# Kernel optimization log

Hardware: AMD Instinct MI355X
Metric: run time of the kernel (lower is better)

The kernel has to match this reference:

```python
import jax, jax.numpy as jnp
import numpy as np
from jax import lax

GAMMA = 0.001  # init kwarg gamma
DN = ('NCHW', 'OIHW', 'NCHW')


def _maxpool2(x):
    # 2x2 max pool, stride 2, NCHW
    return lax.reduce_window(x, -jnp.inf, lax.max, (1, 1, 2, 2), (1, 1, 2, 2), 'VALID')


def _features(x, w1, b1, w2, b2):
    h = lax.conv_general_dilated(x, w1, (1, 1), 'SAME', dimension_numbers=DN)
    h = _maxpool2(jax.nn.relu(h + b1[None, :, None, None]))
    h = lax.conv_general_dilated(h, w2, (1, 1), 'SAME', dimension_numbers=DN)
    h = _maxpool2(jax.nn.relu(h + b2[None, :, None, None]))
    return h.reshape(h.shape[0], -1)  # [N, 16*7*7=784]


def setup_inputs() -> dict:
    key = jax.random.key(0)
    ks = jax.random.split(key, 7)
    x = jax.random.normal(ks[0], (4096, 1, 28, 28), dtype=jnp.float32)
    w1 = jax.random.normal(ks[1], (8, 1, 3, 3), dtype=jnp.float32) * 0.1
    b1 = jax.random.normal(ks[2], (8,), dtype=jnp.float32) * 0.1
    w2 = jax.random.normal(ks[3], (16, 8, 3, 3), dtype=jnp.float32) * 0.1
    b2 = jax.random.normal(ks[4], (16,), dtype=jnp.float32) * 0.1
    support = jax.random.uniform(ks[5], (8192, 784), dtype=jnp.float32)
    alpha = jax.random.normal(ks[6], (8192, 4), dtype=jnp.float32)
    return {'x': x, 'w1': w1, 'b1': b1, 'w2': w2, 'b2': b2,
            'support': support, 'alpha': alpha}


def reference(x, w1, b1, w2, b2, support, alpha):
    feats = _features(x, w1, b1, w2, b2)                      # [N, 784]
    # Pairwise squared distances via expansion (replaces the N*M python loop)
    f2 = jnp.sum(feats * feats, axis=1, keepdims=True)        # [N, 1]
    s2 = jnp.sum(support * support, axis=1)[None, :]          # [1, M]
    d2 = f2 + s2 - 2.0 * (feats @ support.T)                  # [N, M]
    K = jnp.exp(-GAMMA * d2)                                  # RBF kernel matrix
    return K @ alpha                                          # [N, n_classes]
```

## Files before the change

### kernel.cpp

```cpp
#include <hip/hip_runtime.h>
#include <hip/hip_bf16.h>
#include <cstdint>

#define GAMMA 0.001f
#define TILE_BYTES 114688

typedef __attribute__((ext_vector_type(4))) float f32x4;
typedef __attribute__((ext_vector_type(8))) int v8i;
typedef __attribute__((ext_vector_type(8))) short bh8;
typedef unsigned char u8;

__device__ inline unsigned pack4_fp8(float4 f) {
  unsigned p = __builtin_amdgcn_cvt_pk_fp8_f32(f.x, f.y, 0, false);
  p = __builtin_amdgcn_cvt_pk_fp8_f32(f.z, f.w, p, true);
  return p;
}

__device__ inline ushort bf16u(float v) {
  __hip_bfloat16 h = __float2bfloat16(v);
  return *(ushort*)&h;
}

__global__ __launch_bounds__(256, 4) void conv_prep_kernel(
    const float* __restrict__ x, const float* __restrict__ w1,
    const float* __restrict__ b1, const float* __restrict__ w2,
    const float* __restrict__ b2, const float* __restrict__ support,
    const float* __restrict__ alpha, u8* __restrict__ feats_t,
    u8* __restrict__ sup_t, float* __restrict__ beta,
    float* __restrict__ ef) {
  int tid = threadIdx.x;
  int bx = blockIdx.x;

  if (bx >= 2048) {
    int lane = tid & 63, wave = tid >> 6;
    int m = (bx - 2048) * 4 + wave;
    const float* row = support + (size_t)m * 784;
    int mt = m >> 7, mr = m & 127;
    u8* tb = sup_t + (size_t)mt * TILE_BYTES;
    float ss = 0.f;
    if (lane < 56) {
      uint4 w;
      if (lane < 49) {
        float4 f0 = ((const float4*)row)[lane * 4 + 0];
        float4 f1 = ((const float4*)row)[lane * 4 + 1];
        float4 f2 = ((const float4*)row)[lane * 4 + 2];
        float4 f3 = ((const float4*)row)[lane * 4 + 3];
        ss = f0.x * f0.x + f0.y * f0.y + f0.z * f0.z + f0.w * f0.w +
             f1.x * f1.x + f1.y * f1.y + f1.z * f1.z + f1.w * f1.w +
             f2.x * f2.x + f2.y * f2.y + f2.z * f2.z + f2.w * f2.w +
             f3.x * f3.x + f3.y * f3.y + f3.z * f3.z + f3.w * f3.w;
        w.x = pack4_fp8(f0); w.y = pack4_fp8(f1);
        w.z = pack4_fp8(f2); w.w = pack4_fp8(f3);
      } else {
        w.x = 0; w.y = 0; w.z = 0; w.w = 0;
      }
      int kk = lane >> 3, u = lane & 7, q = u >> 1, h = u & 1;
      int qs = q ^ ((mr >> 1) & 3);
      *(uint4*)(tb + kk * 16384 + h * 8192 + mr * 64 + qs * 16) = w;
    }
#pragma unroll
    for (int s = 1; s < 64; s <<= 1) ss += __shfl_xor(ss, s, 64);
    if (lane == 0) {
      float es = __expf(-GAMMA * ss);
      float4 a = ((const float4*)alpha)[m];
      float4 b;
      b.x = es * a.x; b.y = es * a.y; b.z = es * a.z; b.w = es * a.w;
      ((float4*)beta)[m] = b;
    }
    return;
  }

  __shared__ float xp[2][900];
  __shared__ alignas(16) ushort a1h[2][2048];
  __shared__ float w1s[72], b1s[8], b2s[16];
  __shared__ float w2s[1152];
  __shared__ alignas(8) ushort sc[2][16][212];
  __shared__ alignas(16) u8 fb[2][784];
  __shared__ float red[256];

  int lane = tid & 63, wave = tid >> 6;

  for (int t = tid; t < 1800; t += 256) ((float*)xp)[t] = 0.f;
  for (int t = tid; t < 1024; t += 256) ((uint4*)a1h)[t] = (uint4){0, 0, 0, 0};
  if (tid < 72) w1s[tid] = w1[tid];
  if (tid < 8) b1s[tid] = b1[tid];
  if (tid < 16) b2s[tid] = b2[tid];
  for (int t = tid; t < 1152; t += 256) w2s[t] = w2[t];
  __syncthreads();

  int oc = lane & 15, quad = lane >> 4;
  bh8 wf[3];
#pragma unroll
  for (int g = 0; g < 3; g++) {
    int tap = g * 4 + quad;
#pragma unroll
    for (int j = 0; j < 8; j++) {
      float v = (tap < 9) ? w2s[oc * 72 + j * 9 + tap] : 0.f;
      wf[g][j] = (short)bf16u(v);
    }
  }

  for (int t = tid; t < 392; t += 256) {
    int img = t >= 196, j = t - img * 196;
    float4 v = ((const float4*)(x + (size_t)(bx * 2 + img) * 784))[j];
    int r = j / 7, c = (j % 7) * 4;
    float* p = &xp[img][(r + 1) * 30 + (c + 1)];
    p[0] = v.x; p[1] = v.y; p[2] = v.z; p[3] = v.w;
  }
  __syncthreads();

  for (int idx = tid; idx < 3136; idx += 256) {
    int img = idx >= 1568;
    int rem = idx - img * 1568;
    int c = rem / 196, r2 = rem % 196;
    int ph = r2 / 14, pw = r2 % 14;
    const float* w = &w1s[c * 9];
    const float* xb = &xp[img][(2 * ph) * 30 + (2 * pw)];
    float t[4][4];
#pragma unroll
    for (int a = 0; a < 4; a++) {
      float2 u0 = *(const float2*)(xb + a * 30);
      float2 u1 = *(const float2*)(xb + a * 30 + 2);
      t[a][0] = u0.x; t[a][1] = u0.y; t[a][2] = u1.x; t[a][3] = u1.y;
    }
    float s00 = 0, s01 = 0, s10 = 0, s11 = 0;
#pragma unroll
    for (int dy = 0; dy < 3; dy++)
#pragma unroll
      for (int dx = 0; dx < 3; dx++) {
        float wv = w[dy * 3 + dx];
        s00 += t[dy][dx] * wv;     s01 += t[dy][dx + 1] * wv;
        s10 += t[dy + 1][dx] * wv; s11 += t[dy + 1][dx + 1] * wv;
      }
    float mx = fmaxf(fmaxf(s00, s01), fmaxf(s10, s11));
    float val = fmaxf(mx + b1s[c], 0.f);
    a1h[img][((ph + 1) * 16 + (pw + 1)) * 8 + c] = bf16u(val);
  }
  __syncthreads();

  {
    int img2 = wave >> 1, half = wave & 1;
    int Tstart = half * 7, Tcnt = half ? 6 : 7;
    const ushort* abase = a1h[img2];
    int mrow = lane & 15;
    for (int t = 0; t < Tcnt; ++t) {
      int T = Tstart + t;
      int p = T * 16 + mrow;
      int pc = p > 195 ? 195 : p;
      int y = pc / 14, xq = pc - y * 14;
      int cell = y * 16 + xq;
      f32x4 acc = (f32x4){0, 0, 0, 0};
#pragma unroll
      for (int g = 0; g < 3; g++) {
        int tap = g * 4 + quad;
        const ushort* ap;
        if (g == 2 && quad > 0) {
          ap = abase;
        } else {
          int dy = tap / 3, dx = tap - dy * 3;
          ap = abase + (cell + dy * 16 + dx) * 8;
        }
        bh8 af = *(const bh8*)ap;
        acc = __builtin_amdgcn_mfma_f32_16x16x32_bf16(af, wf[g], acc, 0, 0, 0);
      }
      int pos0 = T * 16 + quad * 4;
      ushort4 s4;
      s4.x = bf16u(acc.x); s4.y = bf16u(acc.y);
      s4.z = bf16u(acc.z); s4.w = bf16u(acc.w);
      *(ushort4*)(&sc[img2][oc][pos0]) = s4;
    }
  }
  __syncthreads();

  int img = tid >> 7, r = tid & 127;
  float fsq = 0.f;
  if (r < 112) {
    int o = r & 15, y7 = r >> 4;
    const ushort* srow = sc[img][o];
    float bo = b2s[o];
#pragma unroll
    for (int x7 = 0; x7 < 7; x7++) {
      int p = 28 * y7 + 2 * x7;
      unsigned u0 = *(const unsigned*)(&srow[p]);
      unsigned u1 = *(const unsigned*)(&srow[p + 14]);
      float a = __uint_as_float(u0 << 16);
      float b = __uint_as_float(u0 & 0xffff0000u);
      float c = __uint_as_float(u1 << 16);
      float d = __uint_as_float(u1 & 0xffff0000u);
      float mx = fmaxf(fmaxf(a, b), fmaxf(c, d));
      float val = fmaxf(mx + bo, 0.f);
      fb[img][o * 49 + y7 * 7 + x7] =
          (u8)(__builtin_amdgcn_cvt_pk_fp8_f32(val, 0.f, 0, false) & 0xff);
      fsq += val * val;
    }
  }
  red[tid] = fsq;
  __syncthreads();
  for (int s = 64; s > 0; s >>= 1) {
    if ((tid & 127) < s) red[tid] += red[tid + s];
    __syncthreads();
  }
  if ((tid & 127) == 0) ef[bx * 2 + img] = __expf(-GAMMA * red[tid]);

  if (tid < 112) {
    int im = tid >= 56, j = tid - im * 56;
    uint4 v;
    if (j < 49) v = ((const uint4*)fb[im])[j];
    else { v.x = 0; v.y = 0; v.z = 0; v.w = 0; }
    int n = bx * 2 + im;
    int nt = n >> 7, nr = n & 127;
    int kk = j >> 3, u = j & 7, q = u >> 1, h = u & 1;
    int qs = q ^ ((nr >> 1) & 3);
    *(uint4*)(feats_t + (size_t)nt * TILE_BYTES + kk * 16384 + h * 8192 +
              nr * 64 + qs * 16) = v;
  }
}

__global__ __launch_bounds__(256, 2) void rbf_gemm_kernel(
    const u8* __restrict__ feats_t, const u8* __restrict__ sup_t,
    const float* __restrict__ beta, float* __restrict__ partial) {
  int tid = threadIdx.x;
  int wave = tid >> 6, lane = tid & 63;
  int bx = blockIdx.x;
  int chunk = bx & 63, nb = bx >> 6;
  int wn = wave >> 1, wm = wave & 1;
  int col = lane & 15, quad = lane >> 4;
  int slot = quad ^ ((col >> 1) & 3);

  const u8* abase = feats_t + (size_t)nb * TILE_BYTES +
                    (wn * 64 + col) * 64 + slot * 16;
  const u8* bbase = sup_t + (size_t)chunk * TILE_BYTES +
                    (wm * 64 + col) * 64 + slot * 16;

  f32x4 acc[4][4];
#pragma unroll
  for (int i = 0; i < 4; i++)
#pragma unroll
    for (int j = 0; j < 4; j++) acc[i][j] = (f32x4){0, 0, 0, 0};

#pragma unroll 2
  for (int kk = 0; kk < 7; ++kk) {
    const u8* ak = abase + kk * 16384;
    const u8* bk = bbase + kk * 16384;
    v8i av[4], bv[4];
#pragma unroll
    for (int i = 0; i < 4; i++) {
      const u8* p = ak + i * 1024;
      int4 lo = *(const int4*)p;
      int4 hi = *(const int4*)(p + 8192);
      av[i] = (v8i){lo.x, lo.y, lo.z, lo.w, hi.x, hi.y, hi.z, hi.w};
    }
#pragma unroll
    for (int j = 0; j < 4; j++) {
      const u8* p = bk + j * 1024;
      int4 lo = *(const int4*)p;
      int4 hi = *(const int4*)(p + 8192);
      bv[j] = (v8i){lo.x, lo.y, lo.z, lo.w, hi.x, hi.y, hi.z, hi.w};
    }
#pragma unroll
    for (int i = 0; i < 4; i++)
#pragma unroll
      for (int j = 0; j < 4; j++)
        acc[i][j] = __builtin_amdgcn_mfma_scale_f32_16x16x128_f8f6f4(
            av[i], bv[j], acc[i][j], 0, 0, 0, 0x7f7f7f7f, 0, 0x7f7f7f7f);
  }

#pragma unroll
  for (int i = 0; i < 4; i++)
#pragma unroll
    for (int j = 0; j < 4; j++) {
      acc[i][j].x = __expf(2.f * GAMMA * acc[i][j].x);
      acc[i][j].y = __expf(2.f * GAMMA * acc[i][j].y);
      acc[i][j].z = __expf(2.f * GAMMA * acc[i][j].z);
      acc[i][j].w = __expf(2.f * GAMMA * acc[i][j].w);
    }
  int n0 = nb * 128, m0 = chunk * 128;
#pragma unroll
  for (int c = 0; c < 4; ++c) {
    float bl[4];
#pragma unroll
    for (int j = 0; j < 4; j++)
      bl[j] = beta[(m0 + wm * 64 + j * 16 + col) * 4 + c];
#pragma unroll
    for (int i = 0; i < 4; i++) {
      f32x4 s = acc[i][0] * bl[0] + acc[i][1] * bl[1] + acc[i][2] * bl[2] +
                acc[i][3] * bl[3];
#pragma unroll
      for (int st = 1; st < 16; st <<= 1) {
        s.x += __shfl_xor(s.x, st, 16);
        s.y += __shfl_xor(s.y, st, 16);
        s.z += __shfl_xor(s.z, st, 16);
        s.w += __shfl_xor(s.w, st, 16);
      }
      if (col == c) {
        int n = n0 + wn * 64 + i * 16 + quad * 4;
        float* pp = partial + (((size_t)chunk * 2 + wm) * 4096 + n) * 4 + c;
        pp[0] = s.x; pp[4] = s.y; pp[8] = s.z; pp[12] = s.w;
      }
    }
  }
}

__global__ __launch_bounds__(256) void reduce_kernel(
    const float* __restrict__ partial, const float* __restrict__ ef,
    float* __restrict__ out) {
  __shared__ float4 sred[4][64];
  int nl = threadIdx.x & 63, chq = threadIdx.x >> 6;
  int n = blockIdx.x * 64 + nl;
  const float4* p = (const float4*)partial;
  float sx = 0, sy = 0, sz = 0, sw = 0;
  for (int ch = chq * 32; ch < chq * 32 + 32; ch++) {
    float4 v = p[(size_t)ch * 4096 + n];
    sx += v.x; sy += v.y; sz += v.z; sw += v.w;
  }
  sred[chq][nl] = (float4){sx, sy, sz, sw};
  __syncthreads();
  if (chq == 0) {
    float4 a = sred[0][nl], b = sred[1][nl], c = sred[2][nl], d = sred[3][nl];
    float e = ef[n];
    float4 o;
    o.x = e * (a.x + b.x + c.x + d.x);
    o.y = e * (a.y + b.y + c.y + d.y);
    o.z = e * (a.z + b.z + c.z + d.z);
    o.w = e * (a.w + b.w + c.w + d.w);
    ((float4*)out)[n] = o;
  }
}

extern "C" void kernel_launch(void* const* d_in, const int* in_sizes, int n_in,
                              void* d_out, int out_size, void* d_ws,
                              size_t ws_size, hipStream_t stream) {
  const float* x = (const float*)d_in[0];
  const float* w1 = (const float*)d_in[1];
  const float* b1 = (const float*)d_in[2];
  const float* w2 = (const float*)d_in[3];
  const float* b2 = (const float*)d_in[4];
  const float* support = (const float*)d_in[5];
  const float* alpha = (const float*)d_in[6];
  float* out = (float*)d_out;

  u8* ws = (u8*)d_ws;
  u8* sup_t = ws;
  u8* feats_t = ws + 7340032;
  float* beta = (float*)(ws + 11010048);
  float* ef = (float*)(ws + 11141120);
  float* partial = (float*)(ws + 11157504);

  conv_prep_kernel<<<4096, 256, 0, stream>>>(x, w1, b1, w2, b2, support, alpha,
                                             feats_t, sup_t, beta, ef);
  rbf_gemm_kernel<<<2048, 256, 0, stream>>>(feats_t, sup_t, beta, partial);
  reduce_kernel<<<64, 256, 0, stream>>>(partial, ef, out);
}
```

Measured before the change: 172.0 us.

## Raise GEMM occupancy with staggered fragment loads and widen final reduction

The RBF GEMM kernel's launch bound goes from 2 to 4 blocks per CU and the k-loop is no longer unrolled. A-fragments are now loaded two at a time, interleaved with the MFMAs, which lowers register pressure and lets more waves hide global-load latency. The reduce kernel now uses 256 blocks of 16 rows, each summing 8 chunks per thread group followed by a shared-memory tree reduction, giving more parallelism for the small final pass. The risk is that forcing 4 blocks per CU could cause spills, and dropping the unroll reduces load/compute overlap within a wave.

```diff
diff --git a/kernel.cpp b/kernel.cpp
--- a/kernel.cpp
+++ b/kernel.cpp
@@ -216,7 +216,7 @@
   }
 }
 
-__global__ __launch_bounds__(256, 2) void rbf_gemm_kernel(
+__global__ __launch_bounds__(256, 4) void rbf_gemm_kernel(
     const u8* __restrict__ feats_t, const u8* __restrict__ sup_t,
     const float* __restrict__ beta, float* __restrict__ partial) {
   int tid = threadIdx.x;
@@ -238,32 +238,47 @@
 #pragma unroll
     for (int j = 0; j < 4; j++) acc[i][j] = (f32x4){0, 0, 0, 0};
 
-#pragma unroll 2
+#define LDFRAG(p)                                                      \
+  ({                                                                   \
+    int4 lo_ = *(const int4*)(p);                                      \
+    int4 hi_ = *(const int4*)((p) + 8192);                             \
+    (v8i){lo_.x, lo_.y, lo_.z, lo_.w, hi_.x, hi_.y, hi_.z, hi_.w};     \
+  })
+#define MFMA(a, b, c)                                                  \
+  __builtin_amdgcn_mfma_scale_f32_16x16x128_f8f6f4(                    \
+      (a), (b), (c), 0, 0, 0, 0x7f7f7f7f, 0, 0x7f7f7f7f)
+
+#pragma unroll 1
   for (int kk = 0; kk < 7; ++kk) {
     const u8* ak = abase + kk * 16384;
     const u8* bk = bbase + kk * 16384;
-    v8i av[4], bv[4];
-#pragma unroll
-    for (int i = 0; i < 4; i++) {
-      const u8* p = ak + i * 1024;
-      int4 lo = *(const int4*)p;
-      int4 hi = *(const int4*)(p + 8192);
-      av[i] = (v8i){lo.x, lo.y, lo.z, lo.w, hi.x, hi.y, hi.z, hi.w};
-    }
-#pragma unroll
-    for (int j = 0; j < 4; j++) {
-      const u8* p = bk + j * 1024;
-      int4 lo = *(const int4*)p;
-      int4 hi = *(const int4*)(p + 8192);
-      bv[j] = (v8i){lo.x, lo.y, lo.z, lo.w, hi.x, hi.y, hi.z, hi.w};
-    }
-#pragma unroll
-    for (int i = 0; i < 4; i++)
-#pragma unroll
-      for (int j = 0; j < 4; j++)
-        acc[i][j] = __builtin_amdgcn_mfma_scale_f32_16x16x128_f8f6f4(
-            av[i], bv[j], acc[i][j], 0, 0, 0, 0x7f7f7f7f, 0, 0x7f7f7f7f);
-  }
+    v8i bv0 = LDFRAG(bk);
+    v8i bv1 = LDFRAG(bk + 1024);
+    v8i bv2 = LDFRAG(bk + 2048);
+    v8i bv3 = LDFRAG(bk + 3072);
+    v8i a0 = LDFRAG(ak);
+    v8i a1 = LDFRAG(ak + 1024);
+    acc[0][0] = MFMA(a0, bv0, acc[0][0]);
+    acc[0][1] = MFMA(a0, bv1, acc[0][1]);
+    acc[0][2] = MFMA(a0, bv2, acc[0][2]);
+    acc[0][3] = MFMA(a0, bv3, acc[0][3]);
+    a0 = LDFRAG(ak + 2048);
+    acc[1][0] = MFMA(a1, bv0, acc[1][0]);
+    acc[1][1] = MFMA(a1, bv1, acc[1][1]);
+    acc[1][2] = MFMA(a1, bv2, acc[1][2]);
+    acc[1][3] = MFMA(a1, bv3, acc[1][3]);
+    a1 = LDFRAG(ak + 3072);
+    acc[2][0] = MFMA(a0, bv0, acc[2][0]);
+    acc[2][1] = MFMA(a0, bv1, acc[2][1]);
+    acc[2][2] = MFMA(a0, bv2, acc[2][2]);
+    acc[2][3] = MFMA(a0, bv3, acc[2][3]);
+    acc[3][0] = MFMA(a1, bv0, acc[3][0]);
+    acc[3][1] = MFMA(a1, bv1, acc[3][1]);
+    acc[3][2] = MFMA(a1, bv2, acc[3][2]);
+    acc[3][3] = MFMA(a1, bv3, acc[3][3]);
+  }
+#undef LDFRAG
+#undef MFMA
 
 #pragma unroll
   for (int i = 0; i < 4; i++)
@@ -304,26 +319,29 @@
 __global__ __launch_bounds__(256) void reduce_kernel(
     const float* __restrict__ partial, const float* __restrict__ ef,
     float* __restrict__ out) {
-  __shared__ float4 sred[4][64];
-  int nl = threadIdx.x & 63, chq = threadIdx.x >> 6;
-  int n = blockIdx.x * 64 + nl;
+  __shared__ float4 sred[16][16];
+  int nl = threadIdx.x & 15, sg = threadIdx.x >> 4;
+  int n = blockIdx.x * 16 + nl;
   const float4* p = (const float4*)partial;
   float sx = 0, sy = 0, sz = 0, sw = 0;
-  for (int ch = chq * 32; ch < chq * 32 + 32; ch++) {
+#pragma unroll
+  for (int ch = sg * 8; ch < sg * 8 + 8; ch++) {
     float4 v = p[(size_t)ch * 4096 + n];
     sx += v.x; sy += v.y; sz += v.z; sw += v.w;
   }
-  sred[chq][nl] = (float4){sx, sy, sz, sw};
-  __syncthreads();
-  if (chq == 0) {
-    float4 a = sred[0][nl], b = sred[1][nl], c = sred[2][nl], d = sred[3][nl];
+  sred[sg][nl] = (float4){sx, sy, sz, sw};
+  __syncthreads();
+  for (int st = 8; st > 0; st >>= 1) {
+    if (sg < st) {
+      float4 a = sred[sg][nl], b = sred[sg + st][nl];
+      sred[sg][nl] = (float4){a.x + b.x, a.y + b.y, a.z + b.z, a.w + b.w};
+    }
+    __syncthreads();
+  }
+  if (sg == 0) {
     float e = ef[n];
-    float4 o;
-    o.x = e * (a.x + b.x + c.x + d.x);
-    o.y = e * (a.y + b.y + c.y + d.y);
-    o.z = e * (a.z + b.z + c.z + d.z);
-    o.w = e * (a.w + b.w + c.w + d.w);
-    ((float4*)out)[n] = o;
+    float4 a = sred[0][nl];
+    ((float4*)out)[n] = (float4){e * a.x, e * a.y, e * a.z, e * a.w};
   }
 }
 
@@ -349,5 +367,5 @@
   conv_prep_kernel<<<4096, 256, 0, stream>>>(x, w1, b1, w2, b2, support, alpha,
                                              feats_t, sup_t, beta, ef);
   rbf_gemm_kernel<<<2048, 256, 0, stream>>>(feats_t, sup_t, beta, partial);
-  reduce_kernel<<<64, 256, 0, stream>>>(partial, ef, out);
-}
+  reduce_kernel<<<256, 256, 0, stream>>>(partial, ef, out);
+}
```

Result: faster. 160.3 us (median of 2 runs) (-6.8%).
